# Kernel tuning notes

Hardware: AMD Instinct MI355X
Metric: run time of the kernel (lower is better)

The kernel has to match this reference:

```python
import jax, jax.numpy as jnp
import numpy as np

CLAMP_MAX = float(np.log(100.0))  # temperature clamp from MoELayer


def setup_inputs() -> dict:
    key = jax.random.key(0)
    ks = jax.random.split(key, 4)
    N, D, H, E = 524288, 128, 512, 8
    x = jax.random.normal(ks[0], (N, D), dtype=jnp.float32)
    # per-expert MLP params, stacked along expert axis; scaled like torch Linear init
    W1 = jax.random.normal(ks[1], (E, D, H), dtype=jnp.float32) / np.sqrt(D)
    b1 = jnp.zeros((E, H), dtype=jnp.float32)
    W2 = jax.random.normal(ks[2], (E, H, D), dtype=jnp.float32) / np.sqrt(H)
    b2 = jnp.zeros((E, D), dtype=jnp.float32)
    temperature = jnp.full((1,), np.log(2.0), dtype=jnp.float32)  # init from MoELayer
    return {"x": x, "W1": W1, "b1": b1, "W2": W2, "b2": b2,
            "temperature": temperature}


def reference(x, W1, b1, W2, b2, temperature):
    # Pretraining proportional router: tokens split into E contiguous equal
    # chunks (route_prob == 1), so dispatch/combine is a reshape.
    E = W1.shape[0]
    N, D = x.shape
    xe = x.reshape(E, N // E, D)                      # [E, n, D] dispatched tokens
    h = jax.nn.relu(jnp.einsum('end,edh->enh', xe, W1) + b1[:, None, :])
    y = jnp.einsum('enh,ehd->end', h, W2) + b2[:, None, :]
    logit_scale = jnp.exp(jnp.minimum(temperature, CLAMP_MAX))  # scalar [1]
    out = y.reshape(N, D) * logit_scale
    return out
```

## Files before the change

kernel.cpp:

```cpp
#include <hip/hip_runtime.h>


#define CLAMP_MAXV 4.605170185988091f

typedef __attribute__((ext_vector_type(8))) short s16x8;
typedef __attribute__((ext_vector_type(4))) float f32x4;
typedef __attribute__((ext_vector_type(4))) unsigned short u16x4;
typedef __attribute__((ext_vector_type(8))) unsigned short u16x8;

static __device__ __forceinline__ unsigned short f2bf(float f) {
  union { float f; unsigned int u; } v; v.f = f;
  unsigned int r = v.u + 0x7FFFu + ((v.u >> 16) & 1u);
  return (unsigned short)(r >> 16);
}

static __device__ __forceinline__ void gll16(const void* src, void* dst) {
  __builtin_amdgcn_global_load_lds((const __attribute__((address_space(1))) void*)src,
                                   (__attribute__((address_space(3))) void*)dst, 16, 0, 0);
}

__global__ void conv_w(const float* __restrict__ W1, const float* __restrict__ W2,
                       unsigned short* __restrict__ w1t, unsigned short* __restrict__ w2t) {
  int idx = blockIdx.x * 256 + threadIdx.x;
  if (idx < 65536) {
    int h  = idx & 511;
    int d0 = ((idx >> 9) & 15) << 3;
    int e  = idx >> 13;
    const float* src = W1 + ((size_t)e << 16);
    u16x8 v;
#pragma unroll
    for (int j = 0; j < 8; ++j) v[j] = f2bf(src[(size_t)(d0 + j) * 512 + h]);
    *(u16x8*)(w1t + ((((size_t)e << 9) + h) << 7) + d0) = v;
  } else {
    int i2 = idx - 65536;
    int d  = i2 & 127;
    int h0 = ((i2 >> 7) & 63) << 3;
    int e  = i2 >> 13;
    const float* src = W2 + ((size_t)e << 16);
    u16x8 v;
#pragma unroll
    for (int j = 0; j < 8; ++j) v[j] = f2bf(src[(size_t)(h0 + j) * 128 + d]);
    *(u16x8*)(w2t + ((((size_t)e << 7) + d) << 9) + h0) = v;
  }
}

__global__ __launch_bounds__(512, 4) void moe_fused(
    const float* __restrict__ x,
    const float* __restrict__ b1,
    const float* __restrict__ b2,
    const float* __restrict__ temp,
    const unsigned short* __restrict__ w1t,
    const unsigned short* __restrict__ w2t,
    float* __restrict__ out)
{
  __shared__ __align__(16) char smem[75776];
  char* const xs   = smem;
  char* const w1b0 = smem + 16384;
  char* const w1b1 = smem + 32768;
  char* const w2b  = smem + 49152;
  char* const hsb  = smem + 65536;
  float* const b1s = (float*)(smem + 73728);

  const int tid  = threadIdx.x;
  const int lane = tid & 63;
  const int wid  = tid >> 6;
  const int l15  = lane & 15;
  const int lg   = lane >> 4;
  const int blk  = blockIdx.x;
  const int e    = blk >> 10;

  const int hr  = wid & 3;
  const int tq0 = (wid >> 2) << 5;
  const int tb  = wid & 3;
  const int db  = wid >> 2;

  const unsigned short* w1g = w1t + ((size_t)e << 16);
  const unsigned short* w2g = w2t + ((size_t)e << 16);

  const float* xg = x + ((size_t)blk << 13);
  f32x4 xv[4];
#pragma unroll
  for (int it = 0; it < 4; ++it)
    xv[it] = *(const f32x4*)(xg + ((tid + it * 512) << 2));
  const float b1v   = b1[(e << 9) + tid];
  const float scale = expf(fminf(temp[0], CLAMP_MAXV));

#pragma unroll
  for (int k = 0; k < 2; ++k) {
    int s = tid + (k << 9);
    int hloc = s >> 4, sr = s & 15;
    gll16(w1g + ((size_t)hloc << 7) + ((sr ^ (hloc & 7)) << 3), w1b0 + (s << 4));
  }
#pragma unroll
  for (int k = 0; k < 2; ++k) {
    int s = tid + (k << 9);
    int d = s >> 3, sr = s & 7;
    gll16(w2g + ((size_t)d << 9) + ((sr ^ (d & 7)) << 3), w2b + (s << 4));
  }

#pragma unroll
  for (int it = 0; it < 4; ++it) {
    int idx = (tid + it * 512) << 2;
    int t = idx >> 7, dcol = idx & 127;
    unsigned addr = (unsigned)((t << 8) + (dcol << 1)) ^ (unsigned)((t & 7) << 4);
    u16x4 p;
    p[0] = f2bf(xv[it][0]); p[1] = f2bf(xv[it][1]);
    p[2] = f2bf(xv[it][2]); p[3] = f2bf(xv[it][3]);
    *(u16x4*)(xs + addr) = p;
  }
  b1s[tid] = b1v;

  __syncthreads();

  s16x8 xb[2][4];
#pragma unroll
  for (int j = 0; j < 2; ++j) {
    int tok = tq0 + (j << 4) + l15;
#pragma unroll
    for (int ks = 0; ks < 4; ++ks) {
      unsigned koff = (unsigned)((ks * 32 + lg * 8) << 1);
      xb[j][ks] = *(const s16x8*)(xs + (((unsigned)(tok << 8) + koff) ^ (unsigned)((tok & 7) << 4)));
    }
  }

  f32x4 acc2[4];
#pragma unroll
  for (int j = 0; j < 4; ++j) acc2[j] = (f32x4){0.f, 0.f, 0.f, 0.f};

  const int hrow = hr * 16 + l15;
  const unsigned hswz = (unsigned)((hrow & 7) << 4);
  const int tokr = tb * 16 + l15;
  const unsigned tswz = (unsigned)((tokr & 7) << 4);

#pragma unroll
  for (int c = 0; c < 8; ++c) {
    char* const w1cur = (c & 1) ? w1b1 : w1b0;
    char* const w1nxt = (c & 1) ? w1b0 : w1b1;

    if (c > 0) {
#pragma unroll
      for (int k = 0; k < 2; ++k) {
        int s = tid + (k << 9);
        int d = s >> 3, sr = s & 7;
        gll16(w2g + ((size_t)d << 9) + (c << 6) + ((sr ^ (d & 7)) << 3), w2b + (s << 4));
      }
    }
    if (c < 7) {
#pragma unroll
      for (int k = 0; k < 2; ++k) {
        int s = tid + (k << 9);
        int hloc = s >> 4, sr = s & 15;
        gll16(w1g + ((size_t)((c + 1) * 64 + hloc) << 7) + ((sr ^ (hloc & 7)) << 3),
              w1nxt + (s << 4));
      }
    }

    s16x8 a[4];
#pragma unroll
    for (int ks = 0; ks < 4; ++ks) {
      unsigned koff = (unsigned)((ks * 32 + lg * 8) << 1);
      a[ks] = *(const s16x8*)(w1cur + (((unsigned)(hrow << 8) + koff) ^ hswz));
    }
    f32x4 acc1[2];
    acc1[0] = (f32x4){0.f, 0.f, 0.f, 0.f};
    acc1[1] = (f32x4){0.f, 0.f, 0.f, 0.f};
#pragma unroll
    for (int j = 0; j < 2; ++j)
#pragma unroll
      for (int ks = 0; ks < 4; ++ks)
        acc1[j] = __builtin_amdgcn_mfma_f32_16x16x32_bf16(a[ks], xb[j][ks], acc1[j], 0, 0, 0);

    f32x4 bias = *(const f32x4*)(b1s + c * 64 + hr * 16 + lg * 4);
    const unsigned hl2 = (unsigned)((hr * 16 + lg * 4) << 1);
#pragma unroll
    for (int j = 0; j < 2; ++j) {
      int tok = tq0 + (j << 4) + l15;
      u16x4 p;
#pragma unroll
      for (int r = 0; r < 4; ++r)
        p[r] = f2bf(fmaxf(acc1[j][r] + bias[r], 0.f));
      *(u16x4*)(hsb + (((unsigned)(tok << 7) + hl2) ^ (unsigned)((tok & 7) << 4))) = p;
    }

    __syncthreads();

    s16x8 ha[2];
#pragma unroll
    for (int ks = 0; ks < 2; ++ks) {
      unsigned koff = (unsigned)((ks * 32 + lg * 8) << 1);
      ha[ks] = *(const s16x8*)(hsb + (((unsigned)(tokr << 7) + koff) ^ tswz));
    }
#pragma unroll
    for (int j = 0; j < 4; ++j) {
      int drow = db * 64 + j * 16 + l15;
      unsigned dswz = (unsigned)((drow & 7) << 4);
#pragma unroll
      for (int ks = 0; ks < 2; ++ks) {
        unsigned koff = (unsigned)((ks * 32 + lg * 8) << 1);
        s16x8 wb = *(const s16x8*)(w2b + (((unsigned)(drow << 7) + koff) ^ dswz));
        acc2[j] = __builtin_amdgcn_mfma_f32_16x16x32_bf16(ha[ks], wb, acc2[j], 0, 0, 0);
      }
    }

    if (c < 7) __syncthreads();
  }

  const float* b2e = b2 + (e << 7);
  float* og = out + ((size_t)blk << 13);
#pragma unroll
  for (int j = 0; j < 4; ++j) {
    int d = db * 64 + j * 16 + l15;
    float bv = b2e[d];
#pragma unroll
    for (int r = 0; r < 4; ++r) {
      int t = tb * 16 + lg * 4 + r;
      og[((size_t)t << 7) + d] = (acc2[j][r] + bv) * scale;
    }
  }
}

__global__ void moe_naive(const float* __restrict__ x, const float* __restrict__ W1,
                          const float* __restrict__ b1, const float* __restrict__ W2,
                          const float* __restrict__ b2, const float* __restrict__ temp,
                          float* __restrict__ out) {
  __shared__ float xr[128];
  __shared__ float hrow[512];
  int t = blockIdx.x;
  int e = t >> 16;
  int tx = threadIdx.x;
  xr[tx] = x[((size_t)t << 7) + tx];
  __syncthreads();
  const float* w1e = W1 + ((size_t)e << 16);
  for (int h = tx; h < 512; h += 128) {
    float s = b1[(e << 9) + h];
    for (int d = 0; d < 128; ++d) s += xr[d] * w1e[(size_t)d * 512 + h];
    hrow[h] = fmaxf(s, 0.f);
  }
  __syncthreads();
  const float* w2e = W2 + ((size_t)e << 16);
  float s = b2[(e << 7) + tx];
  for (int h = 0; h < 512; ++h) s += hrow[h] * w2e[(size_t)h * 128 + tx];
  out[((size_t)t << 7) + tx] = s * expf(fminf(temp[0], CLAMP_MAXV));
}

extern "C" void kernel_launch(void* const* d_in, const int* in_sizes, int n_in,
                              void* d_out, int out_size, void* d_ws, size_t ws_size,
                              hipStream_t stream) {
  const float* x    = (const float*)d_in[0];
  const float* W1   = (const float*)d_in[1];
  const float* b1   = (const float*)d_in[2];
  const float* W2   = (const float*)d_in[3];
  const float* b2   = (const float*)d_in[4];
  const float* temp = (const float*)d_in[5];
  float* out = (float*)d_out;

  const size_t WS_NEEDED = 2u * 524288u * sizeof(unsigned short);
  if (ws_size >= WS_NEEDED) {
    unsigned short* w1t = (unsigned short*)d_ws;
    unsigned short* w2t = w1t + 524288;
    conv_w<<<512, 256, 0, stream>>>(W1, W2, w1t, w2t);
    moe_fused<<<8192, 512, 0, stream>>>(x, b1, b2, temp, w1t, w2t, out);
  } else {
    moe_naive<<<524288, 128, 0, stream>>>(x, W1, b1, W2, b2, temp, out);
  }
}
```

Measured before the change: 219.0 us.

## Make fused MoE blocks persistent with resident expert weights in LDS and registers

```diff
diff --git a/kernel.cpp b/kernel.cpp
--- a/kernel.cpp
+++ b/kernel.cpp
@@ -18,6 +18,12 @@
   __builtin_amdgcn_global_load_lds((const __attribute__((address_space(1))) void*)src,
                                    (__attribute__((address_space(3))) void*)dst, 16, 0, 0);
 }
+
+#define LBAR() do { \
+  asm volatile("s_waitcnt lgkmcnt(0)" ::: "memory"); \
+  __builtin_amdgcn_s_barrier(); \
+  __builtin_amdgcn_sched_barrier(0); \
+} while (0)
 
 __global__ void conv_w(const float* __restrict__ W1, const float* __restrict__ W2,
                        unsigned short* __restrict__ w1t, unsigned short* __restrict__ w2t) {
@@ -44,7 +50,7 @@
   }
 }
 
-__global__ __launch_bounds__(512, 4) void moe_fused(
+__global__ __launch_bounds__(512, 2) void moe_fused(
     const float* __restrict__ x,
     const float* __restrict__ b1,
     const float* __restrict__ b2,
@@ -53,13 +59,12 @@
     const unsigned short* __restrict__ w2t,
     float* __restrict__ out)
 {
-  __shared__ __align__(16) char smem[75776];
-  char* const xs   = smem;
-  char* const w1b0 = smem + 16384;
-  char* const w1b1 = smem + 32768;
-  char* const w2b  = smem + 49152;
-  char* const hsb  = smem + 65536;
-  float* const b1s = (float*)(smem + 73728);
+  __shared__ __align__(16) char smem[149504];
+  char* const w1s  = smem;
+  char* const hsb0 = smem + 131072;
+  char* const hsb1 = smem + 139264;
+  char* const xs   = smem + 131072;
+  float* const b1s = (float*)(smem + 147456);
 
   const int tid  = threadIdx.x;
   const int lane = tid & 63;
@@ -67,154 +72,143 @@
   const int l15  = lane & 15;
   const int lg   = lane >> 4;
   const int blk  = blockIdx.x;
-  const int e    = blk >> 10;
+  const int e     = blk >> 7;
+  const int bslot = blk & 127;
+
+  const unsigned short* w1g = w1t + ((size_t)e << 16);
+  const unsigned short* w2g = w2t + ((size_t)e << 16);
+
+#pragma unroll
+  for (int k = 0; k < 16; ++k) {
+    int s = tid + (k << 9);
+    int h = s >> 4, sr = s & 15;
+    gll16(w1g + ((size_t)h << 7) + ((sr ^ (h & 7)) << 3), w1s + (s << 4));
+  }
+
+  const int dlane = (wid << 4) + l15;
+  s16x8 w2f[8][2];
+#pragma unroll
+  for (int c = 0; c < 8; ++c)
+#pragma unroll
+    for (int ks = 0; ks < 2; ++ks)
+      w2f[c][ks] = *(const s16x8*)(w2g + ((size_t)dlane << 9) + (c << 6) + (ks << 5) + (lg << 3));
+
+  b1s[tid] = b1[(e << 9) + tid];
+  const float b2v   = b2[(e << 7) + dlane];
+  const float scale = expf(fminf(temp[0], CLAMP_MAXV));
+
+  const float* xbase = x + (((size_t)e << 16) + ((size_t)bslot << 9)) * 128 / 128 * 128;
+  const float* xb0   = x + ((((size_t)e << 16) + ((size_t)bslot << 9)) << 7) / 128;
+  const float* xg = x + (((size_t)(e << 16) + ((size_t)bslot << 9)) << 7) / 128;
+  (void)xbase; (void)xb0; (void)xg;
+  const size_t tok0 = ((size_t)e << 16) + ((size_t)bslot << 9);
+  const float* xblk = x + (tok0 << 7);
+  float* const oblk = out + (tok0 << 7);
+
+  f32x4 xv[4];
+#pragma unroll
+  for (int it = 0; it < 4; ++it)
+    xv[it] = *(const f32x4*)(xblk + ((tid + (it << 9)) << 2));
+
+  __syncthreads();
 
   const int hr  = wid & 3;
   const int tq0 = (wid >> 2) << 5;
-  const int tb  = wid & 3;
-  const int db  = wid >> 2;
-
-  const unsigned short* w1g = w1t + ((size_t)e << 16);
-  const unsigned short* w2g = w2t + ((size_t)e << 16);
-
-  const float* xg = x + ((size_t)blk << 13);
-  f32x4 xv[4];
-#pragma unroll
-  for (int it = 0; it < 4; ++it)
-    xv[it] = *(const f32x4*)(xg + ((tid + it * 512) << 2));
-  const float b1v   = b1[(e << 9) + tid];
-  const float scale = expf(fminf(temp[0], CLAMP_MAXV));
-
-#pragma unroll
-  for (int k = 0; k < 2; ++k) {
-    int s = tid + (k << 9);
-    int hloc = s >> 4, sr = s & 15;
-    gll16(w1g + ((size_t)hloc << 7) + ((sr ^ (hloc & 7)) << 3), w1b0 + (s << 4));
-  }
-#pragma unroll
-  for (int k = 0; k < 2; ++k) {
-    int s = tid + (k << 9);
-    int d = s >> 3, sr = s & 7;
-    gll16(w2g + ((size_t)d << 9) + ((sr ^ (d & 7)) << 3), w2b + (s << 4));
-  }
-
-#pragma unroll
-  for (int it = 0; it < 4; ++it) {
-    int idx = (tid + it * 512) << 2;
-    int t = idx >> 7, dcol = idx & 127;
-    unsigned addr = (unsigned)((t << 8) + (dcol << 1)) ^ (unsigned)((t & 7) << 4);
-    u16x4 p;
-    p[0] = f2bf(xv[it][0]); p[1] = f2bf(xv[it][1]);
-    p[2] = f2bf(xv[it][2]); p[3] = f2bf(xv[it][3]);
-    *(u16x4*)(xs + addr) = p;
-  }
-  b1s[tid] = b1v;
-
-  __syncthreads();
-
-  s16x8 xb[2][4];
-#pragma unroll
-  for (int j = 0; j < 2; ++j) {
-    int tok = tq0 + (j << 4) + l15;
-#pragma unroll
-    for (int ks = 0; ks < 4; ++ks) {
-      unsigned koff = (unsigned)((ks * 32 + lg * 8) << 1);
-      xb[j][ks] = *(const s16x8*)(xs + (((unsigned)(tok << 8) + koff) ^ (unsigned)((tok & 7) << 4)));
-    }
-  }
-
-  f32x4 acc2[4];
-#pragma unroll
-  for (int j = 0; j < 4; ++j) acc2[j] = (f32x4){0.f, 0.f, 0.f, 0.f};
-
-  const int hrow = hr * 16 + l15;
-  const unsigned hswz = (unsigned)((hrow & 7) << 4);
-  const int tokr = tb * 16 + l15;
-  const unsigned tswz = (unsigned)((tokr & 7) << 4);
-
-#pragma unroll
-  for (int c = 0; c < 8; ++c) {
-    char* const w1cur = (c & 1) ? w1b1 : w1b0;
-    char* const w1nxt = (c & 1) ? w1b0 : w1b1;
-
-    if (c > 0) {
-#pragma unroll
-      for (int k = 0; k < 2; ++k) {
-        int s = tid + (k << 9);
-        int d = s >> 3, sr = s & 7;
-        gll16(w2g + ((size_t)d << 9) + (c << 6) + ((sr ^ (d & 7)) << 3), w2b + (s << 4));
-      }
-    }
-    if (c < 7) {
-#pragma unroll
-      for (int k = 0; k < 2; ++k) {
-        int s = tid + (k << 9);
-        int hloc = s >> 4, sr = s & 15;
-        gll16(w1g + ((size_t)((c + 1) * 64 + hloc) << 7) + ((sr ^ (hloc & 7)) << 3),
-              w1nxt + (s << 4));
-      }
-    }
-
-    s16x8 a[4];
-#pragma unroll
-    for (int ks = 0; ks < 4; ++ks) {
-      unsigned koff = (unsigned)((ks * 32 + lg * 8) << 1);
-      a[ks] = *(const s16x8*)(w1cur + (((unsigned)(hrow << 8) + koff) ^ hswz));
-    }
-    f32x4 acc1[2];
-    acc1[0] = (f32x4){0.f, 0.f, 0.f, 0.f};
-    acc1[1] = (f32x4){0.f, 0.f, 0.f, 0.f};
-#pragma unroll
-    for (int j = 0; j < 2; ++j)
-#pragma unroll
-      for (int ks = 0; ks < 4; ++ks)
-        acc1[j] = __builtin_amdgcn_mfma_f32_16x16x32_bf16(a[ks], xb[j][ks], acc1[j], 0, 0, 0);
-
-    f32x4 bias = *(const f32x4*)(b1s + c * 64 + hr * 16 + lg * 4);
-    const unsigned hl2 = (unsigned)((hr * 16 + lg * 4) << 1);
+  const unsigned hl2 = (unsigned)(((hr << 4) + (lg << 2)) << 1);
+
+#pragma unroll 1
+  for (int t = 0; t < 8; ++t) {
+#pragma unroll
+    for (int it = 0; it < 4; ++it) {
+      int idx = (tid + (it << 9)) << 2;
+      int tk = idx >> 7, col = idx & 127;
+      unsigned addr = (unsigned)((tk << 8) + (col << 1)) ^ (unsigned)((tk & 7) << 4);
+      u16x4 p;
+      p[0] = f2bf(xv[it][0]); p[1] = f2bf(xv[it][1]);
+      p[2] = f2bf(xv[it][2]); p[3] = f2bf(xv[it][3]);
+      *(u16x4*)(xs + addr) = p;
+    }
+    if (t < 7) {
+      const float* xn = xblk + (((size_t)t + 1) << 13);
+#pragma unroll
+      for (int it = 0; it < 4; ++it)
+        xv[it] = *(const f32x4*)(xn + ((tid + (it << 9)) << 2));
+    }
+    LBAR();
+
+    s16x8 xb[2][4];
 #pragma unroll
     for (int j = 0; j < 2; ++j) {
-      int tok = tq0 + (j << 4) + l15;
-      u16x4 p;
-#pragma unroll
-      for (int r = 0; r < 4; ++r)
-        p[r] = f2bf(fmaxf(acc1[j][r] + bias[r], 0.f));
-      *(u16x4*)(hsb + (((unsigned)(tok << 7) + hl2) ^ (unsigned)((tok & 7) << 4))) = p;
-    }
-
-    __syncthreads();
-
-    s16x8 ha[2];
-#pragma unroll
-    for (int ks = 0; ks < 2; ++ks) {
-      unsigned koff = (unsigned)((ks * 32 + lg * 8) << 1);
-      ha[ks] = *(const s16x8*)(hsb + (((unsigned)(tokr << 7) + koff) ^ tswz));
-    }
-#pragma unroll
-    for (int j = 0; j < 4; ++j) {
-      int drow = db * 64 + j * 16 + l15;
-      unsigned dswz = (unsigned)((drow & 7) << 4);
-#pragma unroll
-      for (int ks = 0; ks < 2; ++ks) {
-        unsigned koff = (unsigned)((ks * 32 + lg * 8) << 1);
-        s16x8 wb = *(const s16x8*)(w2b + (((unsigned)(drow << 7) + koff) ^ dswz));
-        acc2[j] = __builtin_amdgcn_mfma_f32_16x16x32_bf16(ha[ks], wb, acc2[j], 0, 0, 0);
-      }
-    }
-
-    if (c < 7) __syncthreads();
-  }
-
-  const float* b2e = b2 + (e << 7);
-  float* og = out + ((size_t)blk << 13);
-#pragma unroll
-  for (int j = 0; j < 4; ++j) {
-    int d = db * 64 + j * 16 + l15;
-    float bv = b2e[d];
-#pragma unroll
-    for (int r = 0; r < 4; ++r) {
-      int t = tb * 16 + lg * 4 + r;
-      og[((size_t)t << 7) + d] = (acc2[j][r] + bv) * scale;
+      int tk = tq0 + (j << 4) + l15;
+#pragma unroll
+      for (int ks = 0; ks < 4; ++ks) {
+        unsigned koff = (unsigned)(((ks << 5) + (lg << 3)) << 1);
+        xb[j][ks] = *(const s16x8*)(xs + (((unsigned)(tk << 8) + koff) ^ (unsigned)((tk & 7) << 4)));
+      }
+    }
+    LBAR();
+
+    f32x4 acc2[4];
+#pragma unroll
+    for (int i = 0; i < 4; ++i) acc2[i] = (f32x4){0.f, 0.f, 0.f, 0.f};
+
+#pragma unroll
+    for (int c = 0; c <= 8; ++c) {
+      if (c < 8) {
+        const int hrow = (c << 6) + (hr << 4) + l15;
+        const unsigned hswz = (unsigned)((hrow & 7) << 4);
+        s16x8 a[4];
+#pragma unroll
+        for (int ks = 0; ks < 4; ++ks) {
+          unsigned koff = (unsigned)(((ks << 5) + (lg << 3)) << 1);
+          a[ks] = *(const s16x8*)(w1s + (((unsigned)(hrow << 8) + koff) ^ hswz));
+        }
+        f32x4 acc1[2];
+        acc1[0] = (f32x4){0.f, 0.f, 0.f, 0.f};
+        acc1[1] = (f32x4){0.f, 0.f, 0.f, 0.f};
+#pragma unroll
+        for (int j = 0; j < 2; ++j)
+#pragma unroll
+          for (int ks = 0; ks < 4; ++ks)
+            acc1[j] = __builtin_amdgcn_mfma_f32_16x16x32_bf16(a[ks], xb[j][ks], acc1[j], 0, 0, 0);
+
+        f32x4 bias = *(const f32x4*)(b1s + (c << 6) + (hr << 4) + (lg << 2));
+        char* const hw = (c & 1) ? hsb1 : hsb0;
+#pragma unroll
+        for (int j = 0; j < 2; ++j) {
+          int tk = tq0 + (j << 4) + l15;
+          u16x4 p;
+#pragma unroll
+          for (int r = 0; r < 4; ++r)
+            p[r] = f2bf(fmaxf(acc1[j][r] + bias[r], 0.f));
+          *(u16x4*)(hw + (((unsigned)(tk << 7) + hl2) ^ (unsigned)((tk & 7) << 4))) = p;
+        }
+      }
+      if (c > 0) {
+        char* const hrd = ((c - 1) & 1) ? hsb1 : hsb0;
+#pragma unroll
+        for (int i = 0; i < 4; ++i) {
+          int tk = (i << 4) + l15;
+          unsigned tswz = (unsigned)((tk & 7) << 4);
+#pragma unroll
+          for (int ks = 0; ks < 2; ++ks) {
+            unsigned koff = (unsigned)(((ks << 5) + (lg << 3)) << 1);
+            s16x8 ha = *(const s16x8*)(hrd + (((unsigned)(tk << 7) + koff) ^ tswz));
+            acc2[i] = __builtin_amdgcn_mfma_f32_16x16x32_bf16(ha, w2f[c - 1][ks], acc2[i], 0, 0, 0);
+          }
+        }
+      }
+      LBAR();
+    }
+
+    float* og = oblk + ((size_t)t << 13);
+#pragma unroll
+    for (int i = 0; i < 4; ++i) {
+#pragma unroll
+      for (int r = 0; r < 4; ++r) {
+        int tk = (i << 4) + (lg << 2) + r;
+        og[((size_t)tk << 7) + dlane] = (acc2[i][r] + b2v) * scale;
+      }
     }
   }
 }
@@ -259,7 +253,7 @@
     unsigned short* w1t = (unsigned short*)d_ws;
     unsigned short* w2t = w1t + 524288;
     conv_w<<<512, 256, 0, stream>>>(W1, W2, w1t, w2t);
-    moe_fused<<<8192, 512, 0, stream>>>(x, b1, b2, temp, w1t, w2t, out);
+    moe_fused<<<1024, 512, 0, stream>>>(x, b1, b2, temp, w1t, w2t, out);
   } else {
     moe_naive<<<524288, 128, 0, stream>>>(x, W1, b1, W2, b2, temp, out);
   }
```

After: 193.6 us. 11.6% less time.
